# Kernel tuning notes

Hardware: AMD Instinct MI355X
Metric: run time of the kernel (lower is better)

The kernel has to match this reference:

```python
import jax, jax.numpy as jnp
import numpy as np
from jax import lax

B, C, H, W = 32, 256, 56, 56
WS = 7            # window size (grid attention: window pixels strided by n1/n2)
NH, DH = 8, 32    # num_head = C // dim_head
EPS = 1e-5        # nn.BatchNorm2d default eps


def _pw(x, w, b):
    # 1x1 conv: (B,C,H,W) x (O,C,1,1) -> (B,O,H,W)
    return jnp.einsum('bchw,oc->bohw', x, w[:, :, 0, 0]) + b[None, :, None, None]


def _dw(x, w, b):
    # depthwise 'same' conv, w: (C,1,k,k)
    k = w.shape[-1]
    p = k // 2
    y = lax.conv_general_dilated(x, w, (1, 1), [(p, p), (p, p)],
                                 dimension_numbers=('NCHW', 'OIHW', 'NCHW'),
                                 feature_group_count=x.shape[1])
    return y + b[None, :, None, None]


def setup_inputs():
    key = jax.random.key(0)
    ks = jax.random.split(key, 8)
    s = 0.05
    return {
        'x': jax.random.normal(ks[0], (B, C, H, W), jnp.float32),
        'bn_gamma': jnp.ones((C,), jnp.float32),
        'bn_beta': jnp.zeros((C,), jnp.float32),
        'qkv_w': jax.random.normal(ks[1], (3 * C, C, 1, 1), jnp.float32) * s,
        'qkv_b': jnp.zeros((3 * C,), jnp.float32),
        'conv3_w': jax.random.normal(ks[2], (C, 1, 3, 3), jnp.float32) * s,
        'conv3_b': jnp.zeros((C,), jnp.float32),
        'conv5_w': jax.random.normal(ks[3], (C, 1, 5, 5), jnp.float32) * s,
        'conv5_b': jnp.zeros((C,), jnp.float32),
        'conv7_w': jax.random.normal(ks[4], (C, 1, 7, 7), jnp.float32) * s,
        'conv7_b': jnp.zeros((C,), jnp.float32),
        'ffn_in_w': jax.random.normal(ks[5], (C, C, 1, 1), jnp.float32) * s,
        'ffn_in_b': jnp.zeros((C,), jnp.float32),
        'conv_local_w': jax.random.normal(ks[6], (C, 1, 3, 3), jnp.float32) * s,
        'conv_local_b': jnp.zeros((C,), jnp.float32),
        'ffn_out_w': jax.random.normal(ks[7], (C, C, 1, 1), jnp.float32) * s,
        'ffn_out_b': jnp.zeros((C,), jnp.float32),
    }


def reference(x, bn_gamma, bn_beta, qkv_w, qkv_b, conv3_w, conv3_b, conv5_w,
              conv5_b, conv7_w, conv7_b, ffn_in_w, ffn_in_b, conv_local_w,
              conv_local_b, ffn_out_w, ffn_out_b):
    # training-mode BatchNorm2d (batch statistics, biased variance)
    mean = x.mean(axis=(0, 2, 3))
    var = x.var(axis=(0, 2, 3))
    xn = bn_gamma[None, :, None, None] * (x - mean[None, :, None, None]) \
         * lax.rsqrt(var + EPS)[None, :, None, None] + bn_beta[None, :, None, None]

    n1, n2 = H // WS, W // WS  # H,W divisible by WS -> pad is a no-op
    # rearrange 'b c (h1 n1) (w1 n2) -> (b n1 n2) c h1 w1' (strided/grid windows)
    xw = xn.reshape(B, C, WS, n1, WS, n2).transpose(0, 3, 5, 1, 2, 4)
    bw = B * n1 * n2
    xw = xw.reshape(bw, C, WS, WS)
    hw = WS * WS

    qkv = _pw(xw, qkv_w, qkv_b)                         # (bw, 3C, WS, WS)
    qkv = qkv.reshape(bw, 3, NH, DH, hw).transpose(1, 0, 2, 4, 3)  # (3,bw,NH,hw,DH)
    q, k, v = qkv[0], qkv[1], qkv[2]
    # v-residual injected before SDPA
    v = v + xw.reshape(bw, NH, DH, hw).transpose(0, 1, 3, 2)

    attn = jax.nn.softmax(jnp.einsum('bnqd,bnkd->bnqk', q, k)
                          / np.float32(np.sqrt(DH)), axis=-1)
    x_spa = jnp.einsum('bnqk,bnkd->bnqd', attn, v)
    x_spa = x_spa.transpose(0, 1, 3, 2).reshape(bw, C, WS, WS)

    # parallel depthwise conv branches, weights all 0.25
    x_spa = 0.25 * (x_spa + _dw(xw, conv3_w, conv3_b)
                    + _dw(xw, conv5_w, conv5_b) + _dw(xw, conv7_w, conv7_b))
    xa = x_spa + v.transpose(0, 1, 3, 2).reshape(bw, C, WS, WS)

    # un-window: '(b n1 n2) c h1 w1 -> b c (h1 n1) (w1 n2)'
    xa = xa.reshape(B, n1, n2, C, WS, WS).transpose(0, 3, 4, 1, 5, 2).reshape(B, C, H, W)

    shortcut = xa
    y = _pw(xa, ffn_in_w, ffn_in_b)
    y = _dw(y, conv_local_w, conv_local_b)
    y = jax.nn.silu(y)
    y = _pw(y, ffn_out_w, ffn_out_b)
    return y + shortcut
```

## Files before the change

### kernel.cpp

```cpp
#include <hip/hip_runtime.h>
#include <hip/hip_bf16.h>

#define NB 32
#define NC 256
#define NHW 3136
#define NA 25690112ull
#define NPW 3328
#define LTS 396

typedef __attribute__((ext_vector_type(8))) short bf16x8;
typedef __attribute__((ext_vector_type(4))) float f32x4;


static __device__ __forceinline__ unsigned short f2bu(float f) {
    union { __hip_bfloat16 h; unsigned short u; } c;
    c.h = __float2bfloat16(f);
    return c.u;
}
static __device__ __forceinline__ float bu2f(unsigned short us) {
    union { unsigned short u; __hip_bfloat16 h; } c;
    c.u = us;
    return __bfloat162float(c.h);
}

__launch_bounds__(256)
__global__ void bn_part(const float* __restrict__ x, float* __restrict__ part)
{
    const int c = blockIdx.x, bq = blockIdx.y;
    const int tid = threadIdx.x;
    float s = 0.f, s2 = 0.f;
    for (int b = bq * 4; b < bq * 4 + 4; ++b) {
        const float4* p = reinterpret_cast<const float4*>(x + ((size_t)b * NC + c) * NHW);
        for (int i = tid; i < 784; i += 256) {
            const float4 v = p[i];
            s += v.x + v.y + v.z + v.w;
            s2 = fmaf(v.x, v.x, s2); s2 = fmaf(v.y, v.y, s2);
            s2 = fmaf(v.z, v.z, s2); s2 = fmaf(v.w, v.w, s2);
        }
    }
    __shared__ float r1[256], r2[256];
    r1[tid] = s; r2[tid] = s2;
    __syncthreads();
    for (int off = 128; off > 0; off >>= 1) {
        if (tid < off) { r1[tid] += r1[tid + off]; r2[tid] += r2[tid + off]; }
        __syncthreads();
    }
    if (tid == 0) {
        part[(c * 8 + bq) * 2] = r1[0];
        part[(c * 8 + bq) * 2 + 1] = r2[0];
    }
}

__launch_bounds__(256)
__global__ void bn_fin(const float* __restrict__ part,
                       const float* __restrict__ gamma, const float* __restrict__ beta,
                       const float* __restrict__ w3, const float* __restrict__ b3,
                       const float* __restrict__ w5, const float* __restrict__ b5,
                       const float* __restrict__ w7, const float* __restrict__ b7,
                       const float* __restrict__ qkvw,
                       const float* __restrict__ fiw, const float* __restrict__ fow,
                       float* __restrict__ ab, float* __restrict__ wcomb,
                       float* __restrict__ bsum, __hip_bfloat16* __restrict__ Wb,
                       __hip_bfloat16* __restrict__ Wfb, __hip_bfloat16* __restrict__ Wob)
{
    const int c = blockIdx.x;
    const int tid = threadIdx.x;

    if (tid < 49) {
        const int ty = tid / 7, tx = tid % 7;
        float wv = w7[c * 49 + tid];
        if (ty >= 1 && ty <= 5 && tx >= 1 && tx <= 5) wv += w5[c * 25 + (ty - 1) * 5 + (tx - 1)];
        if (ty >= 2 && ty <= 4 && tx >= 2 && tx <= 4) wv += w3[c * 9 + (ty - 2) * 3 + (tx - 2)];
        wcomb[c * 49 + tid] = 0.25f * wv;
    }
    if (tid == 63) bsum[c] = 0.25f * (b3[c] + b5[c] + b7[c]);

#pragma unroll
    for (int r = 0; r < 3; ++r) {
        const int o = 3 * c + r;
        Wb[o * 256 + tid] = __float2bfloat16(qkvw[o * 256 + tid]);
    }
    Wfb[c * 256 + tid] = __float2bfloat16(fiw[c * 256 + tid]);
    Wob[c * 256 + tid] = __float2bfloat16(fow[c * 256 + tid]);

    if (tid == 0) {
        float s = 0.f, s2 = 0.f;
#pragma unroll
        for (int q = 0; q < 8; ++q) {
            s += part[(c * 8 + q) * 2];
            s2 += part[(c * 8 + q) * 2 + 1];
        }
        const float inv_n = 1.f / (float)((size_t)NB * NHW);
        const float mean = s * inv_n;
        const float var = s2 * inv_n - mean * mean;
        const float a = gamma[c] / sqrtf(var + 1e-5f);
        ab[c] = a;
        ab[NC + c] = beta[c] - mean * a;
    }
}

__launch_bounds__(256)
__global__ void xnt_make2(const float* __restrict__ x, const float* __restrict__ ab,
                          unsigned short* __restrict__ XNt, unsigned short* __restrict__ XWW)
{
    const int c0 = blockIdx.x * 64;
    const int j1 = blockIdx.y;
    const int b  = blockIdx.z;
    __shared__ unsigned short lt[64 * LTS];
    __shared__ float aa[64], bb[64];
    const int tid = threadIdx.x;
    if (tid < 64) { aa[tid] = ab[c0 + tid]; bb[tid] = ab[256 + c0 + tid]; }
    __syncthreads();

    for (int idx = tid; idx < 6272; idx += 256) {
        const int c = idx / 98, f = idx - 98 * c;
        const int h1 = f / 14, w4 = (f - 14 * h1) * 4;
        const float4 v = *reinterpret_cast<const float4*>(
            &x[((size_t)(b * NC) + c0 + c) * NHW + (h1 * 8 + j1) * 56 + w4]);
        const float a = aa[c], bv = bb[c];
        union { ushort4 u; __hip_bfloat16 h[4]; } pk;
        pk.h[0] = __float2bfloat16(fmaf(a, v.x, bv));
        pk.h[1] = __float2bfloat16(fmaf(a, v.y, bv));
        pk.h[2] = __float2bfloat16(fmaf(a, v.z, bv));
        pk.h[3] = __float2bfloat16(fmaf(a, v.w, bv));
        *reinterpret_cast<ushort4*>(&lt[c * LTS + h1 * 56 + w4]) = pk.u;
    }
    __syncthreads();

    for (int idx = tid; idx < 6656; idx += 256) {
        const int c = idx / 104, r = idx - 104 * c;
        const int j2 = r / 13, q4 = (r - 13 * j2) * 4;
        unsigned short tmp[4];
#pragma unroll
        for (int e = 0; e < 4; ++e) {
            const int p = q4 + e;
            if (p < 49) {
                const int h1p = p / 7, w1 = p - 7 * h1p;
                tmp[e] = lt[c * LTS + h1p * 56 + w1 * 8 + j2];
            } else {
                tmp[e] = 0;
            }
        }
        ushort4 v; v.x = tmp[0]; v.y = tmp[1]; v.z = tmp[2]; v.w = tmp[3];
        *reinterpret_cast<ushort4*>(
            &XWW[((size_t)(b * NC) + c0 + c) * NPW + (j1 * 8 + j2) * 52 + q4]) = v;
    }

    for (int idx = tid; idx < 6272; idx += 256) {
        const int p = idx >> 7;
        const int r = idx & 127;
        const int j2 = r >> 4, c4 = (r & 15) * 4;
        const int h1p = p / 7, w1 = p - 7 * h1p;
        const int px = h1p * 56 + w1 * 8 + j2;
        ushort4 v;
        v.x = lt[(c4 + 0) * LTS + px];
        v.y = lt[(c4 + 1) * LTS + px];
        v.z = lt[(c4 + 2) * LTS + px];
        v.w = lt[(c4 + 3) * LTS + px];
        *reinterpret_cast<ushort4*>(
            &XNt[((size_t)b * NPW + (j1 * 8 + j2) * 52 + p) * 256 + c0 + c4]) = v;
    }
}

__launch_bounds__(256)
__global__ void gemm_qkv_mfma(const unsigned short* __restrict__ XNt,
                              const unsigned short* __restrict__ Wb,
                              const float* __restrict__ bias,
                              unsigned short* __restrict__ QKt,
                              unsigned short* __restrict__ Vb)
{
    __shared__ unsigned short As[128 * 72];
    __shared__ unsigned short Bs[128 * 72];
    const int t = threadIdx.x;
    const int nn0 = blockIdx.x * 128;
    const int o0 = blockIdx.y * 128;
    const int lane = t & 63;
    const int wid = t >> 6;
    const int lr = lane & 15, lg = lane >> 4;
    const int wo = (wid >> 1) * 64;
    const int wn = (wid & 1) * 64;

    f32x4 acc[4][4];
#pragma unroll
    for (int i = 0; i < 4; ++i)
#pragma unroll
        for (int j = 0; j < 4; ++j)
            acc[i][j] = (f32x4){0.f, 0.f, 0.f, 0.f};

    for (int kt = 0; kt < 4; ++kt) {
        const int k0 = kt * 64;
#pragma unroll
        for (int it = 0; it < 4; ++it) {
            const int idx = it * 256 + t;
            const int row = idx >> 3;
            const int k8 = (idx & 7) * 8;
            *reinterpret_cast<uint4*>(&As[row * 72 + k8]) =
                *reinterpret_cast<const uint4*>(&Wb[(size_t)(o0 + row) * 256 + k0 + k8]);
            *reinterpret_cast<uint4*>(&Bs[row * 72 + k8]) =
                *reinterpret_cast<const uint4*>(&XNt[(size_t)(nn0 + row) * 256 + k0 + k8]);
        }
        __syncthreads();
#pragma unroll
        for (int ks = 0; ks < 2; ++ks) {
            const int kk = ks * 32 + lg * 8;
            bf16x8 af[4], bfr[4];
#pragma unroll
            for (int i = 0; i < 4; ++i) {
                af[i]  = *reinterpret_cast<const bf16x8*>(&As[(wo + i * 16 + lr) * 72 + kk]);
                bfr[i] = *reinterpret_cast<const bf16x8*>(&Bs[(wn + i * 16 + lr) * 72 + kk]);
            }
#pragma unroll
            for (int i = 0; i < 4; ++i)
#pragma unroll
                for (int j = 0; j < 4; ++j)
                    acc[i][j] = __builtin_amdgcn_mfma_f32_16x16x32_bf16(
                        af[i], bfr[j], acc[i][j], 0, 0, 0);
        }
        __syncthreads();
    }

    float* Ts = reinterpret_cast<float*>(As);
#pragma unroll
    for (int osub = 0; osub < 4; ++osub) {
        const float4 b4 = *reinterpret_cast<const float4*>(&bias[o0 + wo + osub * 16 + 4 * lg]);
        const int rowb = (wid >> 1) * 16 + 4 * lg;
#pragma unroll
        for (int j = 0; j < 4; ++j) {
            const int col = wn + j * 16 + lr;
            Ts[(rowb + 0) * 132 + col] = acc[osub][j][0] + b4.x;
            Ts[(rowb + 1) * 132 + col] = acc[osub][j][1] + b4.y;
            Ts[(rowb + 2) * 132 + col] = acc[osub][j][2] + b4.z;
            Ts[(rowb + 3) * 132 + col] = acc[osub][j][3] + b4.w;
        }
        __syncthreads();
        if (o0 < 512) {
#pragma unroll
            for (int p = 0; p < 4; ++p) {
                const int item = p * 256 + t;
                const int n = item >> 3;
                const int half = (item >> 2) & 1;
                const int o4 = (item & 3) * 4;
                union { ushort4 u; __hip_bfloat16 h[4]; } pk;
#pragma unroll
                for (int e = 0; e < 4; ++e)
                    pk.h[e] = __float2bfloat16(Ts[(half * 16 + o4 + e) * 132 + n]);
                const int nn = nn0 + n;
                const int bb2 = nn / NPW;
                const int np = nn - bb2 * NPW;
                const int o = o0 + half * 64 + osub * 16 + o4;
                *reinterpret_cast<ushort4*>(&QKt[((size_t)bb2 * NPW + np) * 512 + o]) = pk.u;
            }
        } else {
#pragma unroll
            for (int p = 0; p < 4; ++p) {
                const int idx = p * 256 + t;
                const int row = idx >> 5;
                const int c4 = (idx & 31) * 4;
                const float4 v = *reinterpret_cast<const float4*>(&Ts[row * 132 + c4]);
                const int o = o0 + (row >> 4) * 64 + osub * 16 + (row & 15);
                const int nn = nn0 + c4;
                const int bb2 = nn / NPW;
                const int n = nn - bb2 * NPW;
                union { ushort4 u; __hip_bfloat16 h[4]; } pk;
                pk.h[0] = __float2bfloat16(v.x);
                pk.h[1] = __float2bfloat16(v.y);
                pk.h[2] = __float2bfloat16(v.z);
                pk.h[3] = __float2bfloat16(v.w);
                *reinterpret_cast<ushort4*>(&Vb[((size_t)bb2 * 256 + (o - 512)) * NPW + n]) = pk.u;
            }
        }
        __syncthreads();
    }
}

template<bool RES, bool OUTBF16>
__launch_bounds__(256)
__global__ void gemm_ffn_mfma(const unsigned short* __restrict__ Bt,
                              const unsigned short* __restrict__ Wb2,
                              const float* __restrict__ bias,
                              const float* __restrict__ res, float* __restrict__ outF,
                              unsigned short* __restrict__ outU)
{
    __shared__ unsigned short As[128 * 72];
    __shared__ unsigned short Bs[128 * 72];
    const int t = threadIdx.x;
    const int o0 = blockIdx.x * 128;
    const int nn0 = blockIdx.y * 128;
    const int lane = t & 63;
    const int wid = t >> 6;
    const int lr = lane & 15, lg = lane >> 4;
    const int wo = (wid >> 1) * 64;
    const int wn = (wid & 1) * 64;

    f32x4 acc[4][4];
#pragma unroll
    for (int i = 0; i < 4; ++i)
#pragma unroll
        for (int j = 0; j < 4; ++j)
            acc[i][j] = (f32x4){0.f, 0.f, 0.f, 0.f};

    for (int kt = 0; kt < 4; ++kt) {
        const int k0 = kt * 64;
#pragma unroll
        for (int it = 0; it < 4; ++it) {
            const int idx = it * 256 + t;
            const int row = idx >> 3;
            const int k8 = (idx & 7) * 8;
            *reinterpret_cast<uint4*>(&As[row * 72 + k8]) =
                *reinterpret_cast<const uint4*>(&Wb2[(size_t)(o0 + row) * 256 + k0 + k8]);
            *reinterpret_cast<uint4*>(&Bs[row * 72 + k8]) =
                *reinterpret_cast<const uint4*>(&Bt[(size_t)(nn0 + row) * 256 + k0 + k8]);
        }
        __syncthreads();
#pragma unroll
        for (int ks = 0; ks < 2; ++ks) {
            const int kk = ks * 32 + lg * 8;
            bf16x8 af[4], bfr[4];
#pragma unroll
            for (int i = 0; i < 4; ++i) {
                af[i]  = *reinterpret_cast<const bf16x8*>(&As[(wo + i * 16 + lr) * 72 + kk]);
                bfr[i] = *reinterpret_cast<const bf16x8*>(&Bs[(wn + i * 16 + lr) * 72 + kk]);
            }
#pragma unroll
            for (int i = 0; i < 4; ++i)
#pragma unroll
                for (int j = 0; j < 4; ++j)
                    acc[i][j] = __builtin_amdgcn_mfma_f32_16x16x32_bf16(
                        af[i], bfr[j], acc[i][j], 0, 0, 0);
        }
        __syncthreads();
    }

    float* Ts = reinterpret_cast<float*>(As);
#pragma unroll
    for (int osub = 0; osub < 4; ++osub) {
        const float4 b4 = *reinterpret_cast<const float4*>(&bias[o0 + wo + osub * 16 + 4 * lg]);
        const int rowb = (wid >> 1) * 16 + 4 * lg;
#pragma unroll
        for (int j = 0; j < 4; ++j) {
            const int col = wn + j * 16 + lr;
            Ts[(rowb + 0) * 132 + col] = acc[osub][j][0] + b4.x;
            Ts[(rowb + 1) * 132 + col] = acc[osub][j][1] + b4.y;
            Ts[(rowb + 2) * 132 + col] = acc[osub][j][2] + b4.z;
            Ts[(rowb + 3) * 132 + col] = acc[osub][j][3] + b4.w;
        }
        __syncthreads();
#pragma unroll
        for (int p = 0; p < 4; ++p) {
            const int idx = p * 256 + t;
            const int row = idx >> 5;
            const int c4 = (idx & 31) * 4;
            float4 v = *reinterpret_cast<const float4*>(&Ts[row * 132 + c4]);
            const int o = o0 + (row >> 4) * 64 + osub * 16 + (row & 15);
            const int nn = nn0 + c4;
            const int b2 = nn / NHW;
            const int n = nn - b2 * NHW;
            const size_t po = ((size_t)(b2 * NC + o)) * NHW + n;
            if (OUTBF16) {
                union { ushort4 u; __hip_bfloat16 h[4]; } pk;
                pk.h[0] = __float2bfloat16(v.x);
                pk.h[1] = __float2bfloat16(v.y);
                pk.h[2] = __float2bfloat16(v.z);
                pk.h[3] = __float2bfloat16(v.w);
                *reinterpret_cast<ushort4*>(&outU[po]) = pk.u;
            } else {
                if (RES) {
                    const float4 rv = *reinterpret_cast<const float4*>(&res[po]);
                    v.x += rv.x; v.y += rv.y; v.z += rv.z; v.w += rv.w;
                }
                *reinterpret_cast<float4*>(&outF[po]) = v;
            }
        }
        __syncthreads();
    }
}

__launch_bounds__(64)
__global__ void attn_mfma(const unsigned short* __restrict__ QKt,
                          const unsigned short* __restrict__ Vb,
                          const unsigned short* __restrict__ XWW,
                          const float* __restrict__ wcomb,
                          const float* __restrict__ bsumg,
                          float* __restrict__ xa)
{
    const int j = blockIdx.x;
    const int head = blockIdx.y;
    const int b = blockIdx.z;
    const int c0 = head * 32;
    const int lane = threadIdx.x;
    const int lr = lane & 15, lg = lane >> 4;

    __shared__ __align__(16) char smem[17920];
    unsigned short* P  = (unsigned short*)smem;
    float*          wcl = (float*)smem;
    unsigned short* SP = (unsigned short*)(smem + 6272);
    unsigned short* VT = (unsigned short*)(smem + 10240);
    unsigned short* X  = (unsigned short*)(smem + 14592);

    const size_t qkbase = ((size_t)b * NPW + j * 52) * 512 + c0 + lg * 8;
    uint4 aqr[4], bkr[4];
#pragma unroll
    for (int mi = 0; mi < 4; ++mi) {
        const unsigned short* rp = QKt + qkbase + (size_t)(mi * 16 + lr) * 512;
        aqr[mi] = *reinterpret_cast<const uint4*>(rp);
        bkr[mi] = *reinterpret_cast<const uint4*>(rp + 256);
    }
    const int dd = lane >> 1;
    const int qn = (lane & 1) ? 6 : 7;
    const int qb = (lane & 1) * 7;
    const size_t pbase = ((size_t)(b * NC) + c0 + dd) * NPW + j * 52;
    ushort4 uvr[7], uxr[7];
#pragma unroll
    for (int ii = 0; ii < 7; ++ii)
        if (ii < qn) {
            const int q4 = (qb + ii) * 4;
            uvr[ii] = *reinterpret_cast<const ushort4*>(&Vb[pbase + q4]);
            uxr[ii] = *reinterpret_cast<const ushort4*>(&XWW[pbase + q4]);
        }

    f32x4 acc[4][4];
#pragma unroll
    for (int mi = 0; mi < 4; ++mi)
#pragma unroll
        for (int ni = 0; ni < 4; ++ni)
            acc[mi][ni] = (f32x4){0.f, 0.f, 0.f, 0.f};
    {
        union { uint4 u; bf16x8 v; } ca, cb;
#pragma unroll
        for (int mi = 0; mi < 4; ++mi)
#pragma unroll
            for (int ni = 0; ni < 4; ++ni) {
                ca.u = aqr[mi]; cb.u = bkr[ni];
                acc[mi][ni] = __builtin_amdgcn_mfma_f32_16x16x32_bf16(
                    ca.v, cb.v, acc[mi][ni], 0, 0, 0);
            }
    }

#pragma unroll
    for (int ii = 0; ii < 7; ++ii)
        if (ii < qn) {
            const int q4 = (qb + ii) * 4;
            union { ushort4 u; unsigned short s[4]; } uo;
            const unsigned short* vs = (const unsigned short*)&uvr[ii];
            const unsigned short* xs2 = (const unsigned short*)&uxr[ii];
#pragma unroll
            for (int e = 0; e < 4; ++e) {
                const float vv = bu2f(vs[e]) + bu2f(xs2[e]);
                uo.s[e] = (q4 + e >= 49) ? (unsigned short)0 : f2bu(vv);
            }
            *reinterpret_cast<ushort4*>(&VT[dd * 68 + q4]) = uo.u;
            *reinterpret_cast<ushort4*>(&X[dd * 52 + q4]) = uxr[ii];
        }
    if (lane & 1) {
        ushort4 z; z.x = 0; z.y = 0; z.z = 0; z.w = 0;
        *reinterpret_cast<ushort4*>(&VT[dd * 68 + 52]) = z;
        *reinterpret_cast<ushort4*>(&VT[dd * 68 + 56]) = z;
        *reinterpret_cast<ushort4*>(&VT[dd * 68 + 60]) = z;
    }

    const float sc = 0.17677669529663687f;
#pragma unroll
    for (int mi = 0; mi < 4; ++mi)
#pragma unroll
        for (int reg = 0; reg < 4; ++reg) {
            const float v0 = acc[mi][0][reg] * sc;
            const float v1 = acc[mi][1][reg] * sc;
            const float v2 = acc[mi][2][reg] * sc;
            const float v3 = acc[mi][3][reg] * sc;
            float m = fmaxf(fmaxf(v0, v1), v2);
            if (lr == 0) m = fmaxf(m, v3);
            m = fmaxf(m, __shfl_xor(m, 1));
            m = fmaxf(m, __shfl_xor(m, 2));
            m = fmaxf(m, __shfl_xor(m, 4));
            m = fmaxf(m, __shfl_xor(m, 8));
            const float e0 = __expf(v0 - m), e1 = __expf(v1 - m), e2 = __expf(v2 - m);
            const float e3 = (lr == 0) ? __expf(v3 - m) : 0.f;
            float s = e0 + e1 + e2 + e3;
            s += __shfl_xor(s, 1);
            s += __shfl_xor(s, 2);
            s += __shfl_xor(s, 4);
            s += __shfl_xor(s, 8);
            const float inv = 1.f / s;
            acc[mi][0][reg] = e0 * inv;
            acc[mi][1][reg] = e1 * inv;
            acc[mi][2][reg] = e2 * inv;
            acc[mi][3][reg] = e3 * inv;
        }

#pragma unroll
    for (int mi = 0; mi < 4; ++mi)
#pragma unroll
        for (int ni = 0; ni < 4; ++ni)
#pragma unroll
            for (int reg = 0; reg < 4; ++reg)
                P[(mi * 16 + lg * 4 + reg) * 80 + ni * 16 + lr] = f2bu(acc[mi][ni][reg]);

    f32x4 acc2[4][2];
#pragma unroll
    for (int mi = 0; mi < 4; ++mi)
#pragma unroll
        for (int ni = 0; ni < 2; ++ni)
            acc2[mi][ni] = (f32x4){0.f, 0.f, 0.f, 0.f};
#pragma unroll
    for (int ks = 0; ks < 2; ++ks) {
        bf16x8 ap[4];
#pragma unroll
        for (int mi = 0; mi < 4; ++mi)
            ap[mi] = *reinterpret_cast<const bf16x8*>(&P[(mi * 16 + lr) * 80 + ks * 32 + lg * 8]);
        bf16x8 bv2[2];
#pragma unroll
        for (int ni = 0; ni < 2; ++ni) {
            union { uint2 u[2]; bf16x8 v; } cv;
            cv.u[0] = *reinterpret_cast<const uint2*>(&VT[(ni * 16 + lr) * 68 + ks * 32 + lg * 8]);
            cv.u[1] = *reinterpret_cast<const uint2*>(&VT[(ni * 16 + lr) * 68 + ks * 32 + lg * 8 + 4]);
            bv2[ni] = cv.v;
        }
#pragma unroll
        for (int mi = 0; mi < 4; ++mi)
#pragma unroll
            for (int ni = 0; ni < 2; ++ni)
                acc2[mi][ni] = __builtin_amdgcn_mfma_f32_16x16x32_bf16(
                    ap[mi], bv2[ni], acc2[mi][ni], 0, 0, 0);
    }
    __builtin_amdgcn_sched_barrier(0);

#pragma unroll
    for (int mi = 0; mi < 4; ++mi)
#pragma unroll
        for (int ni = 0; ni < 2; ++ni)
#pragma unroll
            for (int reg = 0; reg < 4; ++reg) {
                const int p = mi * 16 + lg * 4 + reg;
                if (p < 49)
                    SP[(ni * 16 + lr) * 52 + p] = f2bu(acc2[mi][ni][reg]);
            }
    for (int i = lane; i < 392; i += 64)
        *reinterpret_cast<float4*>(&wcl[i * 4]) =
            *reinterpret_cast<const float4*>(&wcomb[c0 * 49 + i * 4]);

    for (int it = 0; it < 4; ++it) {
        const int item = it * 64 + lane;
        if (item < 224) {
            const int d = item / 7, h1 = item - 7 * d;
            const float bsv = bsumg[c0 + d];
            float accw[7];
#pragma unroll
            for (int w1 = 0; w1 < 7; ++w1) {
                const int p = h1 * 7 + w1;
                accw[w1] = fmaf(0.25f, bu2f(SP[d * 52 + p]), bsv + bu2f(VT[d * 68 + p]));
            }
#pragma unroll
            for (int dy = 0; dy < 7; ++dy) {
                const int ry = h1 + dy - 3;
                const bool rok = (ry >= 0) && (ry < 7);
                const int ryc = rok ? ry : 0;
                float xr[7];
#pragma unroll
                for (int i2 = 0; i2 < 7; ++i2) {
                    const float xv = bu2f(X[d * 52 + ryc * 7 + i2]);
                    xr[i2] = rok ? xv : 0.f;
                }
#pragma unroll
                for (int dx = 0; dx < 7; ++dx) {
                    const float wv = wcl[d * 49 + dy * 7 + dx];
#pragma unroll
                    for (int w1 = 0; w1 < 7; ++w1) {
                        const int rx = w1 + dx - 3;
                        if (rx >= 0 && rx < 7) accw[w1] = fmaf(wv, xr[rx], accw[w1]);
                    }
                }
            }
            float* xap = xa + ((size_t)(b * NC + c0 + d)) * NHW + j * 49 + h1 * 7;
#pragma unroll
            for (int w1 = 0; w1 < 7; ++w1) xap[w1] = accw[w1];
        }
    }
}

template<bool F32IN>
__launch_bounds__(256)
__global__ void t256(const float* __restrict__ srcF, const unsigned short* __restrict__ srcU,
                     unsigned short* __restrict__ dst)
{
    const int n0 = blockIdx.x * 64;
    const int b = blockIdx.y;
    __shared__ unsigned short lt[64 * 264];
    const int t = threadIdx.x;
    for (int idx = t; idx < 4096; idx += 256) {
        const int c = idx >> 4, nq = (idx & 15) * 4;
        ushort4 u;
        if (F32IN) {
            const float4 v = *reinterpret_cast<const float4*>(
                &srcF[((size_t)(b * NC) + c) * NHW + n0 + nq]);
            u.x = f2bu(v.x); u.y = f2bu(v.y); u.z = f2bu(v.z); u.w = f2bu(v.w);
        } else {
            u = *reinterpret_cast<const ushort4*>(
                &srcU[((size_t)(b * NC) + c) * NHW + n0 + nq]);
        }
        lt[(nq + 0) * 264 + c] = u.x;
        lt[(nq + 1) * 264 + c] = u.y;
        lt[(nq + 2) * 264 + c] = u.z;
        lt[(nq + 3) * 264 + c] = u.w;
    }
    __syncthreads();
#pragma unroll
    for (int p = 0; p < 16; ++p) {
        const int idx = p * 256 + t;
        const int row = idx >> 6;
        const int c4 = (idx & 63) * 4;
        *reinterpret_cast<ushort4*>(&dst[((size_t)b * NHW + n0 + row) * 256 + c4]) =
            *reinterpret_cast<const ushort4*>(&lt[row * 264 + c4]);
    }
}

__launch_bounds__(256)
__global__ void dw3_silu(const unsigned short* __restrict__ T, const float* __restrict__ wloc,
                         const float* __restrict__ bloc, unsigned short* __restrict__ Uu,
                         float* xa)
{
    const int c = blockIdx.x, b = blockIdx.y;
    const size_t pb = ((size_t)b * NC + c) * NHW;
    __shared__ float pl[56 * 57];
    __shared__ float xpl[3136];
    const int tid = threadIdx.x;
    const ushort4* t4 = reinterpret_cast<const ushort4*>(T + pb);
    const float4* x4 = reinterpret_cast<const float4*>(xa + pb);
    for (int i = tid; i < 784; i += 256) {
        const ushort4 tv = t4[i];
        const float4 xv = x4[i];
        const float tt[4] = {bu2f(tv.x), bu2f(tv.y), bu2f(tv.z), bu2f(tv.w)};
        const float xx[4] = {xv.x, xv.y, xv.z, xv.w};
#pragma unroll
        for (int e = 0; e < 4; ++e) {
            const int n = 4 * i + e;
            const int j = n / 49, p = n - 49 * j;
            const int h1 = p / 7, w1 = p - 7 * h1;
            const int h = h1 * 8 + (j >> 3), w = w1 * 8 + (j & 7);
            pl[h * 57 + w] = tt[e];
            xpl[h * 56 + w] = xx[e];
        }
    }
    __syncthreads();

    float wk[9];
#pragma unroll
    for (int k = 0; k < 9; ++k) wk[k] = wloc[c * 9 + k];
    const float bs = bloc[c];
    unsigned short* up = Uu + pb;
    for (int i4 = tid; i4 < 784; i4 += 256) {
        ushort4 pk;
        unsigned short* pks = (unsigned short*)&pk;
#pragma unroll
        for (int e = 0; e < 4; ++e) {
            const int i = 4 * i4 + e;
            const int h = i / 56, w = i - 56 * h;
            float acc = bs;
#pragma unroll
            for (int dy = -1; dy <= 1; ++dy) {
                const int hh = h + dy;
                if (hh < 0 || hh >= 56) continue;
#pragma unroll
                for (int dx = -1; dx <= 1; ++dx) {
                    const int ww = w + dx;
                    if (ww < 0 || ww >= 56) continue;
                    acc = fmaf(wk[(dy + 1) * 3 + (dx + 1)], pl[hh * 57 + ww], acc);
                }
            }
            pks[e] = f2bu(acc / (1.f + __expf(-acc)));
        }
        *reinterpret_cast<ushort4*>(&up[4 * i4]) = pk;
    }

    float4* xo4 = reinterpret_cast<float4*>(xa + pb);
    for (int i = tid; i < 784; i += 256)
        xo4[i] = make_float4(xpl[4 * i], xpl[4 * i + 1], xpl[4 * i + 2], xpl[4 * i + 3]);
}

extern "C" void kernel_launch(void* const* d_in, const int* in_sizes, int n_in,
                              void* d_out, int out_size, void* d_ws, size_t ws_size,
                              hipStream_t stream)
{
    (void)in_sizes; (void)n_in; (void)out_size; (void)ws_size;
    const float* x    = (const float*)d_in[0];
    const float* g    = (const float*)d_in[1];
    const float* be   = (const float*)d_in[2];
    const float* qkvw = (const float*)d_in[3];
    const float* qkvb = (const float*)d_in[4];
    const float* w3   = (const float*)d_in[5];
    const float* b3   = (const float*)d_in[6];
    const float* w5   = (const float*)d_in[7];
    const float* b5   = (const float*)d_in[8];
    const float* w7   = (const float*)d_in[9];
    const float* b7   = (const float*)d_in[10];
    const float* fiw  = (const float*)d_in[11];
    const float* fib  = (const float*)d_in[12];
    const float* clw  = (const float*)d_in[13];
    const float* clb  = (const float*)d_in[14];
    const float* fow  = (const float*)d_in[15];
    const float* fob  = (const float*)d_in[16];
    float* out = (float*)d_out;

    float* W     = (float*)d_ws;
    float* ab    = W;
    float* wcomb = W + 512;
    float* bsum  = W + 13056;
    float* part  = W + 13312;
    __hip_bfloat16* Wb  = (__hip_bfloat16*)(W + 17408);
    __hip_bfloat16* Wfb = (__hip_bfloat16*)(W + 115712);
    __hip_bfloat16* Wob = (__hip_bfloat16*)(W + 148480);
    float* xa    = W + 181248;
    unsigned short* XNt = (unsigned short*)xa;
    float* R     = xa + NA;
    unsigned short* QKt = (unsigned short*)R;
    unsigned short* Vb  = QKt + (size_t)NB * NPW * 512;
    unsigned short* XWW = Vb + (size_t)NB * 256 * NPW;
    unsigned short* T   = (unsigned short*)R;
    unsigned short* Uu  = T + NA;
    unsigned short* XAt = Vb;
    unsigned short* Ut  = XWW;

    bn_part<<<dim3(256, 8), dim3(256), 0, stream>>>(x, part);
    bn_fin<<<dim3(256), dim3(256), 0, stream>>>(part, g, be, w3, b3, w5, b5, w7, b7,
                                                qkvw, fiw, fow, ab, wcomb, bsum,
                                                Wb, Wfb, Wob);
    xnt_make2<<<dim3(4, 8, NB), dim3(256), 0, stream>>>(x, ab, XNt, XWW);
    gemm_qkv_mfma<<<dim3(832, 6), dim3(256), 0, stream>>>(
        XNt, (const unsigned short*)Wb, qkvb, QKt, Vb);
    attn_mfma<<<dim3(64, 8, NB), dim3(64), 0, stream>>>(
        QKt, Vb, XWW, wcomb, bsum, xa);
    t256<true><<<dim3(49, NB), dim3(256), 0, stream>>>(xa, nullptr, XAt);
    gemm_ffn_mfma<false, true><<<dim3(2, 784), dim3(256), 0, stream>>>(
        XAt, (const unsigned short*)Wfb, fib, nullptr, nullptr, T);
    dw3_silu<<<dim3(256, NB), dim3(256), 0, stream>>>(T, clw, clb, Uu, xa);
    t256<false><<<dim3(49, NB), dim3(256), 0, stream>>>(nullptr, Uu, Ut);
    gemm_ffn_mfma<true, false><<<dim3(2, 784), dim3(256), 0, stream>>>(
        Ut, (const unsigned short*)Wob, fob, xa, out, nullptr);
}
```

Baseline: 792.4 us.

## Fuse transposes into FFN GEMM loads and transpose QK^T softmax layout

Removes the two t256 transpose kernels: the FFN GEMMs now read channel-major activations (fp32 or bf16) directly and transpose them into LDS while staging, converting to bf16 on the fly. This drops a full write and read of two activation-sized intermediates. The attention kernel also swaps the MFMA operand order so each lane holds keys along its registers. Softmax then reduces mostly in-register with only two cross-lane shuffles, and masks invalid keys with -1e30. The new global loads are strided per channel row and the LDS writes are scalar, which may cost some load efficiency.

```diff
diff --git a/kernel.cpp b/kernel.cpp
--- a/kernel.cpp
+++ b/kernel.cpp
@@ -273,9 +273,10 @@
     }
 }
 
-template<bool RES, bool OUTBF16>
+template<bool RES, bool SRCF32>
 __launch_bounds__(256)
-__global__ void gemm_ffn_mfma(const unsigned short* __restrict__ Bt,
+__global__ void gemm_ffn_mfma(const float* __restrict__ BF,
+                              const unsigned short* __restrict__ BU,
                               const unsigned short* __restrict__ Wb2,
                               const float* __restrict__ bias,
                               const float* __restrict__ res, float* __restrict__ outF,
@@ -299,6 +300,12 @@
         for (int j = 0; j < 4; ++j)
             acc[i][j] = (f32x4){0.f, 0.f, 0.f, 0.f};
 
+    const int cl = t & 63;
+    const int nseg = (t >> 6) * 32;
+    const int nnB = nn0 + nseg;
+    const int b2B = nnB / NHW;
+    const int nB = nnB - b2B * NHW;
+
     for (int kt = 0; kt < 4; ++kt) {
         const int k0 = kt * 64;
 #pragma unroll
@@ -308,8 +315,30 @@
             const int k8 = (idx & 7) * 8;
             *reinterpret_cast<uint4*>(&As[row * 72 + k8]) =
                 *reinterpret_cast<const uint4*>(&Wb2[(size_t)(o0 + row) * 256 + k0 + k8]);
-            *reinterpret_cast<uint4*>(&Bs[row * 72 + k8]) =
-                *reinterpret_cast<const uint4*>(&Bt[(size_t)(nn0 + row) * 256 + k0 + k8]);
+        }
+        {
+            unsigned short* bd = &Bs[nseg * 72 + cl];
+            if (SRCF32) {
+                const float* src = BF + ((size_t)(b2B * NC) + k0 + cl) * NHW + nB;
+#pragma unroll
+                for (int q = 0; q < 8; ++q) {
+                    const float4 vv = *reinterpret_cast<const float4*>(src + q * 4);
+                    bd[(q * 4 + 0) * 72] = f2bu(vv.x);
+                    bd[(q * 4 + 1) * 72] = f2bu(vv.y);
+                    bd[(q * 4 + 2) * 72] = f2bu(vv.z);
+                    bd[(q * 4 + 3) * 72] = f2bu(vv.w);
+                }
+            } else {
+                const unsigned short* src = BU + ((size_t)(b2B * NC) + k0 + cl) * NHW + nB;
+#pragma unroll
+                for (int q = 0; q < 8; ++q) {
+                    const ushort4 uu = *reinterpret_cast<const ushort4*>(src + q * 4);
+                    bd[(q * 4 + 0) * 72] = uu.x;
+                    bd[(q * 4 + 1) * 72] = uu.y;
+                    bd[(q * 4 + 2) * 72] = uu.z;
+                    bd[(q * 4 + 3) * 72] = uu.w;
+                }
+            }
         }
         __syncthreads();
 #pragma unroll
@@ -356,7 +385,7 @@
             const int b2 = nn / NHW;
             const int n = nn - b2 * NHW;
             const size_t po = ((size_t)(b2 * NC + o)) * NHW + n;
-            if (OUTBF16) {
+            if (SRCF32) {
                 union { ushort4 u; __hip_bfloat16 h[4]; } pk;
                 pk.h[0] = __float2bfloat16(v.x);
                 pk.h[1] = __float2bfloat16(v.y);
@@ -430,9 +459,9 @@
         for (int mi = 0; mi < 4; ++mi)
 #pragma unroll
             for (int ni = 0; ni < 4; ++ni) {
-                ca.u = aqr[mi]; cb.u = bkr[ni];
+                cb.u = bkr[mi]; ca.u = aqr[ni];
                 acc[mi][ni] = __builtin_amdgcn_mfma_f32_16x16x32_bf16(
-                    ca.v, cb.v, acc[mi][ni], 0, 0, 0);
+                    cb.v, ca.v, acc[mi][ni], 0, 0, 0);
             }
     }
 
@@ -459,41 +488,45 @@
     }
 
     const float sc = 0.17677669529663687f;
-#pragma unroll
-    for (int mi = 0; mi < 4; ++mi)
-#pragma unroll
-        for (int reg = 0; reg < 4; ++reg) {
-            const float v0 = acc[mi][0][reg] * sc;
-            const float v1 = acc[mi][1][reg] * sc;
-            const float v2 = acc[mi][2][reg] * sc;
-            const float v3 = acc[mi][3][reg] * sc;
-            float m = fmaxf(fmaxf(v0, v1), v2);
-            if (lr == 0) m = fmaxf(m, v3);
-            m = fmaxf(m, __shfl_xor(m, 1));
-            m = fmaxf(m, __shfl_xor(m, 2));
-            m = fmaxf(m, __shfl_xor(m, 4));
-            m = fmaxf(m, __shfl_xor(m, 8));
-            const float e0 = __expf(v0 - m), e1 = __expf(v1 - m), e2 = __expf(v2 - m);
-            const float e3 = (lr == 0) ? __expf(v3 - m) : 0.f;
-            float s = e0 + e1 + e2 + e3;
-            s += __shfl_xor(s, 1);
-            s += __shfl_xor(s, 2);
-            s += __shfl_xor(s, 4);
-            s += __shfl_xor(s, 8);
-            const float inv = 1.f / s;
-            acc[mi][0][reg] = e0 * inv;
-            acc[mi][1][reg] = e1 * inv;
-            acc[mi][2][reg] = e2 * inv;
-            acc[mi][3][reg] = e3 * inv;
-        }
-
-#pragma unroll
-    for (int mi = 0; mi < 4; ++mi)
-#pragma unroll
-        for (int ni = 0; ni < 4; ++ni)
+    const int kb = lg * 4;
+#pragma unroll
+    for (int ni = 0; ni < 4; ++ni) {
+        float v[4][4];
+#pragma unroll
+        for (int mi = 0; mi < 4; ++mi)
+#pragma unroll
+            for (int reg = 0; reg < 4; ++reg) {
+                const float raw = acc[mi][ni][reg] * sc;
+                v[mi][reg] = (mi * 16 + kb + reg < 49) ? raw : -1e30f;
+            }
+        float m = -1e30f;
+#pragma unroll
+        for (int mi = 0; mi < 4; ++mi) {
+            const float a0 = fmaxf(v[mi][0], v[mi][1]);
+            const float a1 = fmaxf(v[mi][2], v[mi][3]);
+            m = fmaxf(m, fmaxf(a0, a1));
+        }
+        m = fmaxf(m, __shfl_xor(m, 16));
+        m = fmaxf(m, __shfl_xor(m, 32));
+        float s = 0.f;
+#pragma unroll
+        for (int mi = 0; mi < 4; ++mi)
+#pragma unroll
+            for (int reg = 0; reg < 4; ++reg) {
+                const float e = __expf(v[mi][reg] - m);
+                v[mi][reg] = e;
+                s += e;
+            }
+        s += __shfl_xor(s, 16);
+        s += __shfl_xor(s, 32);
+        const float inv = 1.f / s;
+        unsigned short* Pq = &P[(ni * 16 + lr) * 80];
+#pragma unroll
+        for (int mi = 0; mi < 4; ++mi)
 #pragma unroll
             for (int reg = 0; reg < 4; ++reg)
-                P[(mi * 16 + lg * 4 + reg) * 80 + ni * 16 + lr] = f2bu(acc[mi][ni][reg]);
+                Pq[mi * 16 + kb + reg] = f2bu(v[mi][reg] * inv);
+    }
 
     f32x4 acc2[4][2];
 #pragma unroll
@@ -574,42 +607,6 @@
 #pragma unroll
             for (int w1 = 0; w1 < 7; ++w1) xap[w1] = accw[w1];
         }
-    }
-}
-
-template<bool F32IN>
-__launch_bounds__(256)
-__global__ void t256(const float* __restrict__ srcF, const unsigned short* __restrict__ srcU,
-                     unsigned short* __restrict__ dst)
-{
-    const int n0 = blockIdx.x * 64;
-    const int b = blockIdx.y;
-    __shared__ unsigned short lt[64 * 264];
-    const int t = threadIdx.x;
-    for (int idx = t; idx < 4096; idx += 256) {
-        const int c = idx >> 4, nq = (idx & 15) * 4;
-        ushort4 u;
-        if (F32IN) {
-            const float4 v = *reinterpret_cast<const float4*>(
-                &srcF[((size_t)(b * NC) + c) * NHW + n0 + nq]);
-            u.x = f2bu(v.x); u.y = f2bu(v.y); u.z = f2bu(v.z); u.w = f2bu(v.w);
-        } else {
-            u = *reinterpret_cast<const ushort4*>(
-                &srcU[((size_t)(b * NC) + c) * NHW + n0 + nq]);
-        }
-        lt[(nq + 0) * 264 + c] = u.x;
-        lt[(nq + 1) * 264 + c] = u.y;
-        lt[(nq + 2) * 264 + c] = u.z;
-        lt[(nq + 3) * 264 + c] = u.w;
-    }
-    __syncthreads();
-#pragma unroll
-    for (int p = 0; p < 16; ++p) {
-        const int idx = p * 256 + t;
-        const int row = idx >> 6;
-        const int c4 = (idx & 63) * 4;
-        *reinterpret_cast<ushort4*>(&dst[((size_t)b * NHW + n0 + row) * 256 + c4]) =
-            *reinterpret_cast<const ushort4*>(&lt[row * 264 + c4]);
     }
 }
 
@@ -716,8 +713,6 @@
     unsigned short* XWW = Vb + (size_t)NB * 256 * NPW;
     unsigned short* T   = (unsigned short*)R;
     unsigned short* Uu  = T + NA;
-    unsigned short* XAt = Vb;
-    unsigned short* Ut  = XWW;
 
     bn_part<<<dim3(256, 8), dim3(256), 0, stream>>>(x, part);
     bn_fin<<<dim3(256), dim3(256), 0, stream>>>(part, g, be, w3, b3, w5, b5, w7, b7,
@@ -728,11 +723,9 @@
         XNt, (const unsigned short*)Wb, qkvb, QKt, Vb);
     attn_mfma<<<dim3(64, 8, NB), dim3(64), 0, stream>>>(
         QKt, Vb, XWW, wcomb, bsum, xa);
-    t256<true><<<dim3(49, NB), dim3(256), 0, stream>>>(xa, nullptr, XAt);
     gemm_ffn_mfma<false, true><<<dim3(2, 784), dim3(256), 0, stream>>>(
-        XAt, (const unsigned short*)Wfb, fib, nullptr, nullptr, T);
+        xa, nullptr, (const unsigned short*)Wfb, fib, nullptr, nullptr, T);
     dw3_silu<<<dim3(256, NB), dim3(256), 0, stream>>>(T, clw, clb, Uu, xa);
-    t256<false><<<dim3(49, NB), dim3(256), 0, stream>>>(nullptr, Uu, Ut);
     gemm_ffn_mfma<true, false><<<dim3(2, 784), dim3(256), 0, stream>>>(
-        Ut, (const unsigned short*)Wob, fob, xa, out, nullptr);
-}
+        nullptr, Uu, (const unsigned short*)Wob, fob, xa, out, nullptr);
+}
```

Result: faster. 700.4 us (-11.6%).
